# Kernel optimization log

Measured on AMD Instinct MI355X. Metric: run time of the kernel, lower is better.

The kernel has to match this reference:

```python
import jax, jax.numpy as jnp
import numpy as np

EPS = 1e-6  # kernel_epsilon
NUM_HEADS = 16
NUM_SCALES = 3
ROPE_BASE = 10000.0


def _rope(x, base=ROPE_BASE):
    # x: [B, S, N, D]; rotary applied along seq dim 1 (RotaryPositionEmbedding.forward)
    B, S, N, D = x.shape
    inv_freq = 1.0 / (base ** (jnp.arange(0, D, 2, dtype=jnp.float32) / D))  # [D/2]
    t = jnp.arange(S, dtype=jnp.float32)
    freqs = t[:, None] * inv_freq[None, :]            # [S, D/2]
    emb = jnp.concatenate([freqs, freqs], axis=-1)    # [S, D]
    cos = jnp.cos(emb)[None, :, None, :]
    sin = jnp.sin(emb)[None, :, None, :]
    x1, x2 = jnp.split(x, 2, axis=-1)
    rot = jnp.concatenate([-x2, x1], axis=-1)         # rotate_half
    return x * cos + rot * sin


def _kernel(x):
    # elu kernel: F.elu(x) + 1.0 + epsilon
    return jax.nn.elu(x) + 1.0 + EPS


def setup_inputs() -> dict:
    key = jax.random.key(0)
    ks = jax.random.split(key, 12)
    B, S, H = 4, 2048, 1024
    sc = 1.0 / np.sqrt(H)
    inp = {
        "hidden_states": jax.random.normal(ks[0], (B, S, H), dtype=jnp.float32),
        "attention_mask": jnp.ones((B, S), dtype=jnp.float32),
        "Wq": jax.random.normal(ks[1], (H, H), dtype=jnp.float32) * sc,
        "bq": jnp.zeros((H,), dtype=jnp.float32),
        "Wk": jax.random.normal(ks[2], (H, H), dtype=jnp.float32) * sc,
        "bk": jnp.zeros((H,), dtype=jnp.float32),
        "Wv": jax.random.normal(ks[3], (H, H), dtype=jnp.float32) * sc,
        "bv": jnp.zeros((H,), dtype=jnp.float32),
        "Wo": jax.random.normal(ks[4], (H, H), dtype=jnp.float32) * sc,
        "bo": jnp.zeros((H,), dtype=jnp.float32),
        "Wg": jax.random.normal(ks[5], (H, 1), dtype=jnp.float32) * sc,
        "bg": jnp.zeros((1,), dtype=jnp.float32),  # gate_init_bias = 0.0
        "decay_factors": jnp.ones((NUM_SCALES,), dtype=jnp.float32) * 0.9,
        "gate_weights": jnp.ones((NUM_SCALES,), dtype=jnp.float32) / NUM_SCALES,
    }
    return inp


def reference(hidden_states, attention_mask, Wq, bq, Wk, bk, Wv, bv, Wo, bo,
              Wg, bg, decay_factors, gate_weights):
    B, S, H = hidden_states.shape
    N = NUM_HEADS
    D = H // N
    scaling = D ** -0.5

    q = (hidden_states @ Wq + bq).reshape(B, S, N, D)
    k = (hidden_states @ Wk + bk).reshape(B, S, N, D)
    v = (hidden_states @ Wv + bv).reshape(B, S, N, D)

    # rotary position embeddings on q, k
    q = _rope(q)
    k = _rope(k)

    # kernel feature maps (elu + 1 + eps), query scaling
    q = _kernel(q) * scaling
    k = _kernel(k)

    # apply padding mask to keys/values (mask.unsqueeze(-1).unsqueeze(-1))
    m = attention_mask[:, :, None, None]
    k = k * m
    v = v * m

    # linear (kernelized) attention over the sequence, fused form of
    # einsum('bsnk,bsnv->bsnkv').sum(dim=1)
    kv = jnp.einsum('bsnk,bsnv->bnkv', k, v)          # [B, N, D, D]
    k_sum = jnp.sum(k, axis=1)                        # [B, N, D]
    num = jnp.einsum('bsnk,bnkv->bsnv', q, kv)        # [B, S, N, D]
    den = jnp.einsum('bsnk,bnk->bsn', q, k_sum) + EPS
    attn_out = num / den[..., None]                   # [B, S, N, D]

    # multi-scale memory: starts at zero, one decayed update with this chunk
    decay_sig = jax.nn.sigmoid(decay_factors)                  # [M]
    memory = (1.0 - decay_sig)[None, :, None, None, None] * kv[:, None]  # [B,M,N,D,D]
    mem_scaled = jnp.einsum('bsnk,bmnkv->bmsnv', q, memory)    # [B,M,S,N,D]
    gate_soft = jax.nn.softmax(gate_weights, axis=0)           # [M]
    mem_out = jnp.sum(mem_scaled * gate_soft[None, :, None, None, None], axis=1)

    # sigmoid gate blending local linear attention with memory readout
    g = jax.nn.sigmoid(hidden_states @ Wg + bg)[..., None]     # [B, S, 1, 1]
    combined = g * attn_out + (1.0 - g) * mem_out              # [B, S, N, D]

    out = combined.reshape(B, S, H) @ Wo + bo
    return out
```

## Files before the change

kernel.cpp:

```cpp
#include <hip/hip_runtime.h>
#include <math.h>

#define B_   4
#define S_   2048
#define H_   1024
#define NH   16
#define HD   64
#define T_   (B_ * S_)
#define NCH  16

typedef unsigned short u16;
typedef __bf16 bf16x8 __attribute__((ext_vector_type(8)));
typedef float  f32x4  __attribute__((ext_vector_type(4)));

__device__ __forceinline__ float elu_k(float x) {
    return (x > 0.f ? x : (expf(x) - 1.f)) + 1.000001f;
}

__device__ __forceinline__ u16 f2bf(float x) {
    union { float f; unsigned int u; } v; v.f = x;
    unsigned int r = v.u + 0x7FFFu + ((v.u >> 16) & 1u);
    return (u16)(r >> 16);
}

__device__ __forceinline__ float bfl(unsigned int u) {
    union { unsigned int u; float f; } v; v.u = u << 16; return v.f;
}
__device__ __forceinline__ float bfh(unsigned int u) {
    union { unsigned int u; float f; } v; v.u = u & 0xFFFF0000u; return v.f;
}

__device__ __forceinline__ void async_load16(const u16* g, u16* l) {
    __builtin_amdgcn_global_load_lds(
        (const __attribute__((address_space(1))) void*)g,
        (__attribute__((address_space(3))) void*)l,
        16, 0, 0);
}

__global__ __launch_bounds__(256) void prologue_kernel(
    const float* __restrict__ hs, const float* __restrict__ Wg,
    const float* __restrict__ bg, u16* __restrict__ hsb,
    float* __restrict__ gbuf,
    const float* __restrict__ decay, const float* __restrict__ gate,
    float* __restrict__ coeff, float* __restrict__ cosT,
    float* __restrict__ sinT, const float* __restrict__ bq,
    const float* __restrict__ bk, const float* __restrict__ bv,
    float* __restrict__ bqkv) {
    if (blockIdx.x < T_) {
        int t = blockIdx.x;
        int i = threadIdx.x;
        float4 f = ((const float4*)(hs + (size_t)t * H_))[i];
        float4 w = ((const float4*)Wg)[i];
        ushort4 u;
        u.x = f2bf(f.x); u.y = f2bf(f.y); u.z = f2bf(f.z); u.w = f2bf(f.w);
        ((ushort4*)(hsb + (size_t)t * H_))[i] = u;
        float s = f.x * w.x + f.y * w.y + f.z * w.z + f.w * w.w;
#pragma unroll
        for (int off = 32; off > 0; off >>= 1) s += __shfl_down(s, off);
        __shared__ float wsum[4];
        if ((i & 63) == 0) wsum[i >> 6] = s;
        __syncthreads();
        if (i == 0) {
            float tot = wsum[0] + wsum[1] + wsum[2] + wsum[3];
            gbuf[t] = 1.f / (1.f + expf(-(tot + bg[0])));
        }
        return;
    }
    int idx = (blockIdx.x - T_) * 256 + threadIdx.x;
    if (idx < S_ * 32) {
        int s = idx >> 5, i = idx & 31;
        float inv = powf(10000.f, -(2.f * (float)i) / 64.f);
        float f = (float)s * inv;
        cosT[idx] = cosf(f);
        sinT[idx] = sinf(f);
    } else if (idx < S_ * 32 + 3072) {
        int i = idx - S_ * 32;
        bqkv[i] = (i < 1024) ? bq[i] : (i < 2048) ? bk[i - 1024] : bv[i - 2048];
    } else if (idx == S_ * 32 + 3072) {
        float g0 = gate[0], g1 = gate[1], g2 = gate[2];
        float mx = fmaxf(g0, fmaxf(g1, g2));
        float e0 = expf(g0 - mx), e1 = expf(g1 - mx), e2 = expf(g2 - mx);
        float inv = 1.f / (e0 + e1 + e2);
        float es[3] = {e0, e1, e2};
        float c = 0.f;
        for (int m = 0; m < 3; m++) {
            float ds = 1.f / (1.f + expf(-decay[m]));
            c += es[m] * inv * (1.f - ds);
        }
        *coeff = c;
    }
}

__global__ __launch_bounds__(256) void pack_w_kernel(
    const float* __restrict__ Wq, const float* __restrict__ Wk,
    const float* __restrict__ Wv, const float* __restrict__ Wo,
    u16* __restrict__ Wt) {
    __shared__ u16 tile[64][65];
    const float* W = (blockIdx.z == 0) ? Wq :
                     (blockIdx.z == 1) ? Wk :
                     (blockIdx.z == 2) ? Wv : Wo;
    int nt = blockIdx.x * 64, kt = blockIdx.y * 64;
    int tid = threadIdx.x;
#pragma unroll
    for (int it = 0; it < 16; it++) {
        int i = it * 256 + tid;
        int kr = i >> 6, nc = i & 63;
        tile[kr][nc] = f2bf(W[(size_t)(kt + kr) * H_ + nt + nc]);
    }
    __syncthreads();
    size_t wbase = (size_t)blockIdx.z * H_;
#pragma unroll
    for (int it = 0; it < 16; it++) {
        int i = it * 256 + tid;
        int nr = i >> 6, kc = i & 63;
        Wt[(wbase + nt + nr) * H_ + kt + kc] = tile[kc][nr];
    }
}

#define GEMM_KLOOP(A_, Bt_, bm_, bn_)                                         \
    for (int k0 = 0; k0 < K; k0 += 32) {                                      \
        _Pragma("unroll")                                                     \
        for (int i = 0; i < 4; i++) {                                         \
            int r0 = wave * 64 + i * 16;                                      \
            async_load16(&A_[(size_t)(bm_ + r0 + (lane >> 2)) * K + k0 + (lane & 3) * 8], \
                         &Asl[r0 * 32]);                                      \
        }                                                                     \
        _Pragma("unroll")                                                     \
        for (int i = 0; i < 2; i++) {                                         \
            int r0 = wave * 32 + i * 16;                                      \
            async_load16(&Bt_[(size_t)(bn_ + r0 + (lane >> 2)) * K + k0 + (lane & 3) * 8], \
                         &Bsl[r0 * 32]);                                      \
        }                                                                     \
        asm volatile("s_waitcnt vmcnt(0)" ::: "memory");                      \
        __syncthreads();                                                      \
        bf16x8 bfr[4];                                                        \
        _Pragma("unroll")                                                     \
        for (int nj = 0; nj < 4; nj++)                                        \
            bfr[nj] = *(const bf16x8*)&Bsl[(wn + nj * 16 + l15) * 32 + quad * 8]; \
        _Pragma("unroll")                                                     \
        for (int mi = 0; mi < 8; mi++) {                                      \
            bf16x8 a = *(const bf16x8*)&Asl[(wm + mi * 16 + l15) * 32 + quad * 8]; \
            _Pragma("unroll")                                                 \
            for (int nj = 0; nj < 4; nj++)                                    \
                acc[mi][nj] = __builtin_amdgcn_mfma_f32_16x16x32_bf16(        \
                    a, bfr[nj], acc[mi][nj], 0, 0, 0);                        \
        }                                                                     \
        __syncthreads();                                                      \
    }

__global__ __launch_bounds__(256, 2) void gemm_qkv_kernel(
    const u16* __restrict__ A, const u16* __restrict__ Bt,
    const float* __restrict__ bias, const float* __restrict__ mask,
    const float* __restrict__ cosT, const float* __restrict__ sinT,
    u16* __restrict__ qb, u16* __restrict__ kb, u16* __restrict__ vb) {
    constexpr int K = 1024;
    __shared__ u16 Asl[256 * 32];
    __shared__ u16 Bsl[128 * 32];
    const int tid  = threadIdx.x;
    const int wave = tid >> 6, lane = tid & 63;
    const int wm = (wave & 1) * 128, wn = (wave >> 1) * 64;
    const int bm = blockIdx.y * 256, bn = blockIdx.x * 128;
    const int l15 = lane & 15, quad = lane >> 4;

    f32x4 acc[8][4];
#pragma unroll
    for (int i = 0; i < 8; i++)
#pragma unroll
        for (int j = 0; j < 4; j++) acc[i][j] = {0.f, 0.f, 0.f, 0.f};

    GEMM_KLOOP(A, Bt, bm, bn)

    const int colbase = bn + wn;
    const int region  = colbase >> 10;
    const int n       = (colbase & 1023) >> 6;
    float bc[4];
#pragma unroll
    for (int nj = 0; nj < 4; nj++) bc[nj] = bias[colbase + nj * 16 + l15];
    u16* outp = (region == 0) ? qb : (region == 1) ? kb : vb;

#pragma unroll
    for (int mi = 0; mi < 8; mi++) {
#pragma unroll
        for (int r = 0; r < 4; r++) {
            int row = bm + wm + mi * 16 + quad * 4 + r;
            int b = row >> 11, s = row & (S_ - 1);
            size_t obase = ((size_t)(b * 16 + n) * S_ + s) * 64;
            if (region < 2) {
                float mfac = (region == 0) ? 0.125f : mask[row];
#pragma unroll
                for (int p = 0; p < 2; p++) {
                    int d1 = p * 16 + l15;
                    float c  = cosT[s * 32 + d1];
                    float sn = sinT[s * 32 + d1];
                    float x1 = acc[mi][p][r]     + bc[p];
                    float x2 = acc[mi][p + 2][r] + bc[p + 2];
                    float r1 = x1 * c - x2 * sn;
                    float r2 = x2 * c + x1 * sn;
                    outp[obase + d1]      = f2bf(elu_k(r1) * mfac);
                    outp[obase + d1 + 32] = f2bf(elu_k(r2) * mfac);
                }
            } else {
                float mfac = mask[row];
#pragma unroll
                for (int nj = 0; nj < 4; nj++)
                    outp[obase + nj * 16 + l15] =
                        f2bf((acc[mi][nj][r] + bc[nj]) * mfac);
            }
        }
    }
}

__global__ __launch_bounds__(256, 2) void gemm_out_kernel(
    const u16* __restrict__ A, const u16* __restrict__ Bt,
    const float* __restrict__ bias, float* __restrict__ C, int N) {
    constexpr int K = 1024;
    __shared__ u16 Asl[256 * 32];
    __shared__ u16 Bsl[128 * 32];
    const int tid  = threadIdx.x;
    const int wave = tid >> 6, lane = tid & 63;
    const int wm = (wave & 1) * 128, wn = (wave >> 1) * 64;
    const int bm = blockIdx.y * 256, bn = blockIdx.x * 128;
    const int l15 = lane & 15, quad = lane >> 4;

    f32x4 acc[8][4];
#pragma unroll
    for (int i = 0; i < 8; i++)
#pragma unroll
        for (int j = 0; j < 4; j++) acc[i][j] = {0.f, 0.f, 0.f, 0.f};

    GEMM_KLOOP(A, Bt, bm, bn)

#pragma unroll
    for (int mi = 0; mi < 8; mi++) {
#pragma unroll
        for (int nj = 0; nj < 4; nj++) {
            int col = bn + wn + nj * 16 + l15;
            float bcol = bias[col];
#pragma unroll
            for (int r = 0; r < 4; r++) {
                int row = bm + wm + mi * 16 + quad * 4 + r;
                C[(size_t)row * N + col] = acc[mi][nj][r] + bcol;
            }
        }
    }
}

__global__ __launch_bounds__(256) void kv_part_kernel(
    const u16* __restrict__ kb, const u16* __restrict__ vb,
    float* __restrict__ kvpart, float* __restrict__ kspart) {
    int bn = blockIdx.x;
    const int rows = S_ / NCH;
    int s0 = blockIdx.y * rows;
    int tid = threadIdx.x;
    int ti = tid >> 4, tj = tid & 15;
    __shared__ float ks[16][64], vs[16][64];
    float acc[4][4] = {};
    float ksacc = 0.f;
    const u16* kbase = kb + (size_t)bn * (S_ * 64) + (size_t)s0 * 64;
    const u16* vbase = vb + (size_t)bn * (S_ * 64) + (size_t)s0 * 64;
    for (int ss = 0; ss < rows; ss += 16) {
        {
            int half = tid >> 7;
            int c = tid & 127;
            int rr = c >> 3, col = (c & 7) * 8;
            const u16* src = (half ? vbase : kbase) + (size_t)(ss + rr) * 64 + col;
            uint4 raw = *(const uint4*)src;
            float* dst = half ? &vs[rr][col] : &ks[rr][col];
            dst[0] = bfl(raw.x); dst[1] = bfh(raw.x);
            dst[2] = bfl(raw.y); dst[3] = bfh(raw.y);
            dst[4] = bfl(raw.z); dst[5] = bfh(raw.z);
            dst[6] = bfl(raw.w); dst[7] = bfh(raw.w);
        }
        __syncthreads();
#pragma unroll
        for (int r = 0; r < 16; r++) {
            float a[4], bb[4];
#pragma unroll
            for (int i = 0; i < 4; i++) a[i] = ks[r][ti * 4 + i];
#pragma unroll
            for (int j = 0; j < 4; j++) bb[j] = vs[r][tj * 4 + j];
#pragma unroll
            for (int i = 0; i < 4; i++)
#pragma unroll
                for (int j = 0; j < 4; j++)
                    acc[i][j] = fmaf(a[i], bb[j], acc[i][j]);
        }
        if (tid < 64) {
#pragma unroll
            for (int r = 0; r < 16; r++) ksacc += ks[r][tid];
        }
        __syncthreads();
    }
    size_t obase = ((size_t)blockIdx.y * 64 + bn) * 4096;
#pragma unroll
    for (int i = 0; i < 4; i++)
#pragma unroll
        for (int j = 0; j < 4; j++)
            kvpart[obase + (size_t)(ti * 4 + i) * 64 + tj * 4 + j] = acc[i][j];
    if (tid < 64)
        kspart[((size_t)blockIdx.y * 64 + bn) * 64 + tid] = ksacc;
}

__global__ __launch_bounds__(256) void reduce_part_kernel(
    const float* __restrict__ kvpart, const float* __restrict__ kspart,
    float* __restrict__ kvb, float* __restrict__ ksum) {
    int i = blockIdx.x * 256 + threadIdx.x;
    if (i < 262144) {
        float s = 0.f;
#pragma unroll
        for (int c = 0; c < NCH; c++) s += kvpart[(size_t)c * 262144 + i];
        kvb[i] = s;
    } else if (i < 262144 + 4096) {
        int j = i - 262144;
        float s = 0.f;
#pragma unroll
        for (int c = 0; c < NCH; c++) s += kspart[(size_t)c * 4096 + j];
        ksum[j] = s;
    }
}

__global__ __launch_bounds__(256) void combine_kernel(
    const u16* __restrict__ qb, const float* __restrict__ kvb,
    const float* __restrict__ ksum, const float* __restrict__ g,
    const float* __restrict__ coeffp, u16* __restrict__ cmb) {
    int bn = blockIdx.x;
    int b = bn >> 4, n = bn & 15;
    __shared__ u16 qs[256 * 72];
    __shared__ u16 kvT[64 * 72];
    __shared__ u16 ksl[128];
    int tid = threadIdx.x;
    int s0 = blockIdx.y * 256;

    const u16* qsrc = qb + (size_t)bn * (S_ * 64) + (size_t)s0 * 64;
    for (int c = tid; c < 2048; c += 256) {
        int t = c >> 3, k8 = (c & 7) * 8;
        float4 tmp = *(const float4*)(qsrc + (size_t)c * 8);
        *(float4*)&qs[t * 72 + k8] = tmp;
    }
    for (int c = tid; c < 1024; c += 256) {
        int i = c >> 4, d4 = (c & 15) * 4;
        float4 kvv = *(const float4*)&kvb[(size_t)bn * 4096 + i * 64 + d4];
        kvT[(d4 + 0) * 72 + i] = f2bf(kvv.x);
        kvT[(d4 + 1) * 72 + i] = f2bf(kvv.y);
        kvT[(d4 + 2) * 72 + i] = f2bf(kvv.z);
        kvT[(d4 + 3) * 72 + i] = f2bf(kvv.w);
    }
    if (tid < 64)        ksl[tid] = f2bf(ksum[bn * 64 + tid]);
    else if (tid < 128)  ksl[tid] = 0;
    __syncthreads();

    int wave = tid >> 6, lane = tid & 63;
    int l15 = lane & 15, quad = lane >> 4;
    int wt = wave * 64;

    int ko0 = (l15 == 0) ? quad * 8      : 64;
    int ko1 = (l15 == 0) ? 32 + quad * 8 : 64;
    bf16x8 ksf0 = *(const bf16x8*)&ksl[ko0];
    bf16x8 ksf1 = *(const bf16x8*)&ksl[ko1];

    bf16x8 bfr0[4], bfr1[4];
#pragma unroll
    for (int nj = 0; nj < 4; nj++) {
        bfr0[nj] = *(const bf16x8*)&kvT[(nj * 16 + l15) * 72 + quad * 8];
        bfr1[nj] = *(const bf16x8*)&kvT[(nj * 16 + l15) * 72 + 32 + quad * 8];
    }

    f32x4 acc[4][4], dacc[4];
#pragma unroll
    for (int i = 0; i < 4; i++) {
        dacc[i] = {0.f, 0.f, 0.f, 0.f};
#pragma unroll
        for (int j = 0; j < 4; j++) acc[i][j] = {0.f, 0.f, 0.f, 0.f};
    }

#pragma unroll
    for (int mi = 0; mi < 4; mi++) {
        bf16x8 a0 = *(const bf16x8*)&qs[(wt + mi * 16 + l15) * 72 + quad * 8];
        bf16x8 a1 = *(const bf16x8*)&qs[(wt + mi * 16 + l15) * 72 + 32 + quad * 8];
        dacc[mi] = __builtin_amdgcn_mfma_f32_16x16x32_bf16(a0, ksf0, dacc[mi], 0, 0, 0);
        dacc[mi] = __builtin_amdgcn_mfma_f32_16x16x32_bf16(a1, ksf1, dacc[mi], 0, 0, 0);
#pragma unroll
        for (int nj = 0; nj < 4; nj++) {
            acc[mi][nj] = __builtin_amdgcn_mfma_f32_16x16x32_bf16(
                a0, bfr0[nj], acc[mi][nj], 0, 0, 0);
            acc[mi][nj] = __builtin_amdgcn_mfma_f32_16x16x32_bf16(
                a1, bfr1[nj], acc[mi][nj], 0, 0, 0);
        }
    }

    float coeff = *coeffp;
#pragma unroll
    for (int mi = 0; mi < 4; mi++) {
#pragma unroll
        for (int r = 0; r < 4; r++) {
            int s = s0 + wt + mi * 16 + quad * 4 + r;
            int t = b * S_ + s;
            float den = __shfl(dacc[mi][r], lane & 48) + 1e-6f;
            float gv = g[t];
            float w1 = gv / den + (1.f - gv) * coeff;
#pragma unroll
            for (int nj = 0; nj < 4; nj++) {
                int d = nj * 16 + l15;
                cmb[(size_t)t * H_ + n * 64 + d] = f2bf(acc[mi][nj][r] * w1);
            }
        }
    }
}

extern "C" void kernel_launch(void* const* d_in, const int* in_sizes, int n_in,
                              void* d_out, int out_size, void* d_ws, size_t ws_size,
                              hipStream_t stream) {
    const float* hs    = (const float*)d_in[0];
    const float* mask  = (const float*)d_in[1];
    const float* Wq    = (const float*)d_in[2];
    const float* bq    = (const float*)d_in[3];
    const float* Wk    = (const float*)d_in[4];
    const float* bk    = (const float*)d_in[5];
    const float* Wv    = (const float*)d_in[6];
    const float* bv    = (const float*)d_in[7];
    const float* Wo    = (const float*)d_in[8];
    const float* bo    = (const float*)d_in[9];
    const float* Wg    = (const float*)d_in[10];
    const float* bg    = (const float*)d_in[11];
    const float* decay = (const float*)d_in[12];
    const float* gate  = (const float*)d_in[13];
    float* out = (float*)d_out;

    float* ws     = (float*)d_ws;
    float* kvb    = ws;
    float* ksum   = kvb + 262144;
    float* gbuf   = ksum + 4096;
    float* coeff  = gbuf + 8192;
    float* cosT   = coeff + 64;
    float* sinT   = cosT + 65536;
    float* bqkv   = sinT + 65536;
    float* kspart = bqkv + 4096;
    float* kvpart = kspart + 65536;
    u16*   hsb    = (u16*)(kvpart + 4194304);
    u16*   Wt     = hsb + (size_t)T_ * H_;
    u16*   WoT    = Wt + (size_t)3072 * H_;
    u16*   qb     = Wt + (size_t)4096 * H_;
    u16*   kb     = qb + (size_t)T_ * H_;
    u16*   vb     = kb + (size_t)T_ * H_;
    u16*   cmb    = vb + (size_t)T_ * H_;

    prologue_kernel<<<T_ + (S_ * 32 + 3072 + 256) / 256 + 1, 256, 0, stream>>>(
        hs, Wg, bg, hsb, gbuf, decay, gate, coeff, cosT, sinT, bq, bk, bv, bqkv);
    pack_w_kernel<<<dim3(16, 16, 4), 256, 0, stream>>>(Wq, Wk, Wv, Wo, Wt);

    gemm_qkv_kernel<<<dim3(3072 / 128, T_ / 256), 256, 0, stream>>>(
        hsb, Wt, bqkv, mask, cosT, sinT, qb, kb, vb);

    kv_part_kernel<<<dim3(B_ * NH, NCH), 256, 0, stream>>>(
        kb, vb, kvpart, kspart);
    reduce_part_kernel<<<(262144 + 4096 + 255) / 256, 256, 0, stream>>>(
        kvpart, kspart, kvb, ksum);

    combine_kernel<<<dim3(B_ * NH, S_ / 256), 256, 0, stream>>>(
        qb, kvb, ksum, gbuf, coeff, cmb);

    gemm_out_kernel<<<dim3(H_ / 128, T_ / 256), 256, 0, stream>>>(
        cmb, WoT, bo, out, H_);
}
```

Baseline: 292.0 us.

## Shrink GEMM tiles to 64x128, split prologue, vectorize weight packing

Reduces the QKV and output GEMM block tile from 256x128 to 64x128, with fewer accumulators per wave and more blocks. Splits the hidden-state conversion and gate computation into its own kernel that processes eight tokens per block. Vectorizes the weight transpose/pack with float4 loads and ushort4 stores. The smaller tile raises occupancy but lowers data reuse and the MFMA-to-sync ratio per K step.

```diff
diff --git a/kernel.cpp b/kernel.cpp
--- a/kernel.cpp
+++ b/kernel.cpp
@@ -37,36 +37,13 @@
         16, 0, 0);
 }
 
-__global__ __launch_bounds__(256) void prologue_kernel(
-    const float* __restrict__ hs, const float* __restrict__ Wg,
-    const float* __restrict__ bg, u16* __restrict__ hsb,
-    float* __restrict__ gbuf,
+__global__ __launch_bounds__(256) void prep_kernel(
     const float* __restrict__ decay, const float* __restrict__ gate,
     float* __restrict__ coeff, float* __restrict__ cosT,
     float* __restrict__ sinT, const float* __restrict__ bq,
     const float* __restrict__ bk, const float* __restrict__ bv,
     float* __restrict__ bqkv) {
-    if (blockIdx.x < T_) {
-        int t = blockIdx.x;
-        int i = threadIdx.x;
-        float4 f = ((const float4*)(hs + (size_t)t * H_))[i];
-        float4 w = ((const float4*)Wg)[i];
-        ushort4 u;
-        u.x = f2bf(f.x); u.y = f2bf(f.y); u.z = f2bf(f.z); u.w = f2bf(f.w);
-        ((ushort4*)(hsb + (size_t)t * H_))[i] = u;
-        float s = f.x * w.x + f.y * w.y + f.z * w.z + f.w * w.w;
-#pragma unroll
-        for (int off = 32; off > 0; off >>= 1) s += __shfl_down(s, off);
-        __shared__ float wsum[4];
-        if ((i & 63) == 0) wsum[i >> 6] = s;
-        __syncthreads();
-        if (i == 0) {
-            float tot = wsum[0] + wsum[1] + wsum[2] + wsum[3];
-            gbuf[t] = 1.f / (1.f + expf(-(tot + bg[0])));
-        }
-        return;
-    }
-    int idx = (blockIdx.x - T_) * 256 + threadIdx.x;
+    int idx = blockIdx.x * 256 + threadIdx.x;
     if (idx < S_ * 32) {
         int s = idx >> 5, i = idx & 31;
         float inv = powf(10000.f, -(2.f * (float)i) / 64.f);
@@ -91,80 +68,114 @@
     }
 }
 
+__global__ __launch_bounds__(256) void cvt_gate_kernel(
+    const float* __restrict__ hs, const float* __restrict__ Wg,
+    const float* __restrict__ bg, u16* __restrict__ hsb,
+    float* __restrict__ gbuf) {
+    int tid = threadIdx.x;
+    float4 w = ((const float4*)Wg)[tid];
+    float bgv = bg[0];
+    __shared__ float wsum[4];
+    for (int tt = 0; tt < 8; tt++) {
+        int t = blockIdx.x * 8 + tt;
+        float4 f = ((const float4*)(hs + (size_t)t * H_))[tid];
+        ushort4 u;
+        u.x = f2bf(f.x); u.y = f2bf(f.y); u.z = f2bf(f.z); u.w = f2bf(f.w);
+        ((ushort4*)(hsb + (size_t)t * H_))[tid] = u;
+        float s = f.x * w.x + f.y * w.y + f.z * w.z + f.w * w.w;
+#pragma unroll
+        for (int off = 32; off > 0; off >>= 1) s += __shfl_down(s, off);
+        if ((tid & 63) == 0) wsum[tid >> 6] = s;
+        __syncthreads();
+        if (tid == 0) {
+            float tot = wsum[0] + wsum[1] + wsum[2] + wsum[3];
+            gbuf[t] = 1.f / (1.f + expf(-(tot + bgv)));
+        }
+        __syncthreads();
+    }
+}
+
 __global__ __launch_bounds__(256) void pack_w_kernel(
     const float* __restrict__ Wq, const float* __restrict__ Wk,
     const float* __restrict__ Wv, const float* __restrict__ Wo,
     u16* __restrict__ Wt) {
-    __shared__ u16 tile[64][65];
+    __shared__ u16 tile[64][68];
     const float* W = (blockIdx.z == 0) ? Wq :
                      (blockIdx.z == 1) ? Wk :
                      (blockIdx.z == 2) ? Wv : Wo;
     int nt = blockIdx.x * 64, kt = blockIdx.y * 64;
     int tid = threadIdx.x;
 #pragma unroll
-    for (int it = 0; it < 16; it++) {
+    for (int it = 0; it < 4; it++) {
         int i = it * 256 + tid;
-        int kr = i >> 6, nc = i & 63;
-        tile[kr][nc] = f2bf(W[(size_t)(kt + kr) * H_ + nt + nc]);
+        int kr = i >> 4, nc4 = (i & 15) * 4;
+        float4 f = *(const float4*)&W[(size_t)(kt + kr) * H_ + nt + nc4];
+        tile[kr][nc4 + 0] = f2bf(f.x);
+        tile[kr][nc4 + 1] = f2bf(f.y);
+        tile[kr][nc4 + 2] = f2bf(f.z);
+        tile[kr][nc4 + 3] = f2bf(f.w);
     }
     __syncthreads();
     size_t wbase = (size_t)blockIdx.z * H_;
 #pragma unroll
-    for (int it = 0; it < 16; it++) {
+    for (int it = 0; it < 4; it++) {
         int i = it * 256 + tid;
-        int nr = i >> 6, kc = i & 63;
-        Wt[(wbase + nt + nr) * H_ + kt + kc] = tile[kc][nr];
+        int nr = i >> 4, kc4 = (i & 15) * 4;
+        ushort4 o;
+        o.x = tile[kc4 + 0][nr];
+        o.y = tile[kc4 + 1][nr];
+        o.z = tile[kc4 + 2][nr];
+        o.w = tile[kc4 + 3][nr];
+        *(ushort4*)&Wt[(wbase + nt + nr) * H_ + kt + kc4] = o;
     }
 }
 
 #define GEMM_KLOOP(A_, Bt_, bm_, bn_)                                         \
     for (int k0 = 0; k0 < K; k0 += 32) {                                      \
-        _Pragma("unroll")                                                     \
-        for (int i = 0; i < 4; i++) {                                         \
-            int r0 = wave * 64 + i * 16;                                      \
-            async_load16(&A_[(size_t)(bm_ + r0 + (lane >> 2)) * K + k0 + (lane & 3) * 8], \
-                         &Asl[r0 * 32]);                                      \
-        }                                                                     \
-        _Pragma("unroll")                                                     \
-        for (int i = 0; i < 2; i++) {                                         \
-            int r0 = wave * 32 + i * 16;                                      \
-            async_load16(&Bt_[(size_t)(bn_ + r0 + (lane >> 2)) * K + k0 + (lane & 3) * 8], \
-                         &Bsl[r0 * 32]);                                      \
+        {                                                                     \
+            int rr = lane >> 2, cc = (lane & 3) * 8;                          \
+            async_load16(&A_[(size_t)(bm_ + wave * 16 + rr) * K + k0 + cc],   \
+                         &Asl[(wave * 16) * 32]);                             \
+            async_load16(&Bt_[(size_t)(bn_ + wave * 16 + rr) * K + k0 + cc],  \
+                         &Bsl[(wave * 16) * 32]);                             \
+            async_load16(&Bt_[(size_t)(bn_ + 64 + wave * 16 + rr) * K + k0 + cc], \
+                         &Bsl[(64 + wave * 16) * 32]);                        \
         }                                                                     \
         asm volatile("s_waitcnt vmcnt(0)" ::: "memory");                      \
         __syncthreads();                                                      \
-        bf16x8 bfr[4];                                                        \
+        bf16x8 af[2], bfr[4];                                                 \
+        _Pragma("unroll")                                                     \
+        for (int mi = 0; mi < 2; mi++)                                        \
+            af[mi] = *(const bf16x8*)&Asl[(wm + mi * 16 + l15) * 32 + quad * 8]; \
         _Pragma("unroll")                                                     \
         for (int nj = 0; nj < 4; nj++)                                        \
             bfr[nj] = *(const bf16x8*)&Bsl[(wn + nj * 16 + l15) * 32 + quad * 8]; \
         _Pragma("unroll")                                                     \
-        for (int mi = 0; mi < 8; mi++) {                                      \
-            bf16x8 a = *(const bf16x8*)&Asl[(wm + mi * 16 + l15) * 32 + quad * 8]; \
+        for (int mi = 0; mi < 2; mi++)                                        \
             _Pragma("unroll")                                                 \
             for (int nj = 0; nj < 4; nj++)                                    \
                 acc[mi][nj] = __builtin_amdgcn_mfma_f32_16x16x32_bf16(        \
-                    a, bfr[nj], acc[mi][nj], 0, 0, 0);                        \
-        }                                                                     \
+                    af[mi], bfr[nj], acc[mi][nj], 0, 0, 0);                   \
         __syncthreads();                                                      \
     }
 
-__global__ __launch_bounds__(256, 2) void gemm_qkv_kernel(
+__global__ __launch_bounds__(256) void gemm_qkv_kernel(
     const u16* __restrict__ A, const u16* __restrict__ Bt,
     const float* __restrict__ bias, const float* __restrict__ mask,
     const float* __restrict__ cosT, const float* __restrict__ sinT,
     u16* __restrict__ qb, u16* __restrict__ kb, u16* __restrict__ vb) {
     constexpr int K = 1024;
-    __shared__ u16 Asl[256 * 32];
+    __shared__ u16 Asl[64 * 32];
     __shared__ u16 Bsl[128 * 32];
     const int tid  = threadIdx.x;
     const int wave = tid >> 6, lane = tid & 63;
-    const int wm = (wave & 1) * 128, wn = (wave >> 1) * 64;
-    const int bm = blockIdx.y * 256, bn = blockIdx.x * 128;
+    const int wm = (wave & 1) * 32, wn = (wave >> 1) * 64;
+    const int bm = blockIdx.y * 64, bn = blockIdx.x * 128;
     const int l15 = lane & 15, quad = lane >> 4;
 
-    f32x4 acc[8][4];
-#pragma unroll
-    for (int i = 0; i < 8; i++)
+    f32x4 acc[2][4];
+#pragma unroll
+    for (int i = 0; i < 2; i++)
 #pragma unroll
         for (int j = 0; j < 4; j++) acc[i][j] = {0.f, 0.f, 0.f, 0.f};
 
@@ -179,7 +190,7 @@
     u16* outp = (region == 0) ? qb : (region == 1) ? kb : vb;
 
 #pragma unroll
-    for (int mi = 0; mi < 8; mi++) {
+    for (int mi = 0; mi < 2; mi++) {
 #pragma unroll
         for (int r = 0; r < 4; r++) {
             int row = bm + wm + mi * 16 + quad * 4 + r;
@@ -210,28 +221,28 @@
     }
 }
 
-__global__ __launch_bounds__(256, 2) void gemm_out_kernel(
+__global__ __launch_bounds__(256) void gemm_out_kernel(
     const u16* __restrict__ A, const u16* __restrict__ Bt,
     const float* __restrict__ bias, float* __restrict__ C, int N) {
     constexpr int K = 1024;
-    __shared__ u16 Asl[256 * 32];
+    __shared__ u16 Asl[64 * 32];
     __shared__ u16 Bsl[128 * 32];
     const int tid  = threadIdx.x;
     const int wave = tid >> 6, lane = tid & 63;
-    const int wm = (wave & 1) * 128, wn = (wave >> 1) * 64;
-    const int bm = blockIdx.y * 256, bn = blockIdx.x * 128;
+    const int wm = (wave & 1) * 32, wn = (wave >> 1) * 64;
+    const int bm = blockIdx.y * 64, bn = blockIdx.x * 128;
     const int l15 = lane & 15, quad = lane >> 4;
 
-    f32x4 acc[8][4];
-#pragma unroll
-    for (int i = 0; i < 8; i++)
+    f32x4 acc[2][4];
+#pragma unroll
+    for (int i = 0; i < 2; i++)
 #pragma unroll
         for (int j = 0; j < 4; j++) acc[i][j] = {0.f, 0.f, 0.f, 0.f};
 
     GEMM_KLOOP(A, Bt, bm, bn)
 
 #pragma unroll
-    for (int mi = 0; mi < 8; mi++) {
+    for (int mi = 0; mi < 2; mi++) {
 #pragma unroll
         for (int nj = 0; nj < 4; nj++) {
             int col = bn + wn + nj * 16 + l15;
@@ -444,11 +455,12 @@
     u16*   vb     = kb + (size_t)T_ * H_;
     u16*   cmb    = vb + (size_t)T_ * H_;
 
-    prologue_kernel<<<T_ + (S_ * 32 + 3072 + 256) / 256 + 1, 256, 0, stream>>>(
-        hs, Wg, bg, hsb, gbuf, decay, gate, coeff, cosT, sinT, bq, bk, bv, bqkv);
+    prep_kernel<<<(S_ * 32 + 3072 + 256) / 256 + 1, 256, 0, stream>>>(
+        decay, gate, coeff, cosT, sinT, bq, bk, bv, bqkv);
+    cvt_gate_kernel<<<T_ / 8, 256, 0, stream>>>(hs, Wg, bg, hsb, gbuf);
     pack_w_kernel<<<dim3(16, 16, 4), 256, 0, stream>>>(Wq, Wk, Wv, Wo, Wt);
 
-    gemm_qkv_kernel<<<dim3(3072 / 128, T_ / 256), 256, 0, stream>>>(
+    gemm_qkv_kernel<<<dim3(3072 / 128, T_ / 64), 256, 0, stream>>>(
         hsb, Wt, bqkv, mask, cosT, sinT, qb, kb, vb);
 
     kv_part_kernel<<<dim3(B_ * NH, NCH), 256, 0, stream>>>(
@@ -459,6 +471,6 @@
     combine_kernel<<<dim3(B_ * NH, S_ / 256), 256, 0, stream>>>(
         qb, kvb, ksum, gbuf, coeff, cmb);
 
-    gemm_out_kernel<<<dim3(H_ / 128, T_ / 256), 256, 0, stream>>>(
+    gemm_out_kernel<<<dim3(H_ / 128, T_ / 64), 256, 0, stream>>>(
         cmb, WoT, bo, out, H_);
 }
```

Result: faster. 278.1 us (-4.8%).
